# Kernel tuning notes

Hardware: AMD Instinct MI355X
Metric: run time of the kernel (lower is better)

The kernel has to match this reference:

```python
import jax, jax.numpy as jnp
import numpy as np

TEMPERATURE = 0.07
EPS = 1e-12  # F.normalize eps

B, D = 4096, 512

def setup_inputs() -> dict:
    key = jax.random.key(0)
    k1, k2, k3 = jax.random.split(key, 3)
    z1 = jax.random.normal(k1, (B, D), dtype=jnp.float32)
    z2 = jax.random.normal(k2, (B, D), dtype=jnp.float32)
    labels = jax.random.randint(k3, (B,), 0, 10)
    return {"z1": z1, "z2": z2, "labels": labels}

def _normalize(x):
    # F.normalize(x, dim=1): x / max(||x||, eps)
    n = jnp.linalg.norm(x, axis=1, keepdims=True)
    return x / jnp.maximum(n, EPS)

def reference(z1, z2, labels):
    z1 = _normalize(z1)
    z2 = _normalize(z2)
    batch_size = z1.shape[0]
    features = jnp.concatenate([z1, z2], axis=0)  # [2B, D], unit-norm rows
    # cosine similarity of unit vectors == dot product
    similarity = jnp.einsum('id,jd->ij', features, features) / TEMPERATURE  # [2B,2B]
    # positive mask: (i, i+B) and (i+B, i)
    idx = jnp.arange(2 * batch_size)
    pos_idx = jnp.where(idx < batch_size, idx + batch_size, idx - batch_size)
    # log-softmax over rows (diagonal NOT masked, matching the original)
    log_prob = similarity - jax.nn.logsumexp(similarity, axis=1, keepdims=True)
    pos_log_prob = log_prob[idx, pos_idx]  # [2B]
    loss = -jnp.sum(pos_log_prob) / (2 * batch_size)
    return loss
```

## Files before the change

kernel.cpp:

```cpp
#include <hip/hip_runtime.h>
#include <hip/hip_bf16.h>

#define BSZ   4096
#define DIM   512
#define NROW  8192
#define NBLK_NORM (BSZ / 4)
#define INV_T 14.285714285714285f

typedef float f32x4 __attribute__((ext_vector_type(4)));

#define GLOAD_LDS16(gp, lp) __builtin_amdgcn_global_load_lds( \
    (const __attribute__((address_space(1))) unsigned int*)(const void*)(gp), \
    (__attribute__((address_space(3))) unsigned int*)(void*)(lp), 16, 0, 0)

__device__ __forceinline__ unsigned pack_fp8x4(float4 v, float s) {
    int w = 0;
    w = __builtin_amdgcn_cvt_pk_fp8_f32(v.x * s, v.y * s, w, false);
    w = __builtin_amdgcn_cvt_pk_fp8_f32(v.z * s, v.w * s, w, true);
    return (unsigned)w;
}

__global__ __launch_bounds__(256) void nt_norm(const float* __restrict__ z1,
                                               const float* __restrict__ z2,
                                               unsigned char* __restrict__ F,
                                               float* __restrict__ posbuf,
                                               float* __restrict__ rowsum) {
    __shared__ float pd[4];
    const int wid  = threadIdx.x >> 6;
    const int lane = threadIdx.x & 63;
    const int row  = blockIdx.x * 4 + wid;

    if (threadIdx.x < 8) rowsum[blockIdx.x * 8 + threadIdx.x] = 0.0f;

    const float4* a4 = (const float4*)(z1 + (size_t)row * DIM);
    const float4* b4 = (const float4*)(z2 + (size_t)row * DIM);
    float4 a0 = a4[lane], a1 = a4[64 + lane];
    float4 b0 = b4[lane], b1 = b4[64 + lane];

    float s1 = a0.x*a0.x + a0.y*a0.y + a0.z*a0.z + a0.w*a0.w
             + a1.x*a1.x + a1.y*a1.y + a1.z*a1.z + a1.w*a1.w;
    float s2 = b0.x*b0.x + b0.y*b0.y + b0.z*b0.z + b0.w*b0.w
             + b1.x*b1.x + b1.y*b1.y + b1.z*b1.z + b1.w*b1.w;
    float d  = a0.x*b0.x + a0.y*b0.y + a0.z*b0.z + a0.w*b0.w
             + a1.x*b1.x + a1.y*b1.y + a1.z*b1.z + a1.w*b1.w;

    #pragma unroll
    for (int off = 32; off; off >>= 1) {
        s1 += __shfl_xor(s1, off);
        s2 += __shfl_xor(s2, off);
        d  += __shfl_xor(d,  off);
    }

    const float inv1 = 1.0f / fmaxf(sqrtf(s1), 1e-12f);
    const float inv2 = 1.0f / fmaxf(sqrtf(s2), 1e-12f);

    unsigned char* F1 = F + (size_t)row * DIM;
    unsigned char* F2 = F + (size_t)(BSZ + row) * DIM;
    *(unsigned*)(F1 + lane * 4)       = pack_fp8x4(a0, inv1);
    *(unsigned*)(F1 + 256 + lane * 4) = pack_fp8x4(a1, inv1);
    *(unsigned*)(F2 + lane * 4)       = pack_fp8x4(b0, inv2);
    *(unsigned*)(F2 + 256 + lane * 4) = pack_fp8x4(b1, inv2);

    if (lane == 0) pd[wid] = d * inv1 * inv2;
    __syncthreads();
    if (threadIdx.x == 0)
        posbuf[blockIdx.x] = pd[0] + pd[1] + pd[2] + pd[3];
}

__device__ __forceinline__ void stage_fp8(const unsigned char* __restrict__ Ag,
                                          const unsigned char* __restrict__ Bg,
                                          unsigned char* Asb, unsigned char* Bsb,
                                          int tid, int wid) {
    #pragma unroll
    for (int ch = 0; ch < 4; ++ch) {
        const int i   = ch * 256 + tid;
        const int rr  = i >> 3;
        const int cb  = (i & 7) * 16;
        const int src = cb ^ ((rr & 7) << 4);
        const int seg = (ch * 256 + wid * 64) * 16;
        GLOAD_LDS16(Ag + (size_t)rr * DIM + src, Asb + seg);
        GLOAD_LDS16(Bg + (size_t)rr * DIM + src, Bsb + seg);
    }
}

__global__ __launch_bounds__(256, 4) void simexp(const unsigned char* __restrict__ F,
                                                 float* __restrict__ rowsum) {
    __shared__ __align__(16) unsigned char As[2][128 * 128];
    __shared__ __align__(16) unsigned char Bs[2][128 * 128];

    int L = (blockIdx.x & 7) * 260 + (blockIdx.x >> 3);
    int rem = L, s_r = 0;
    for (; s_r < 8; ++s_r) {
        const int rowsz = 36 + 64 * (7 - s_r);
        if (rem < rowsz) break;
        rem -= rowsz;
    }
    int s_c, lr, lc;
    if (rem < 36) {
        s_c = s_r;
        lr = 0;
        while (rem >= 8 - lr) { rem -= 8 - lr; ++lr; }
        lc = lr + rem;
    } else {
        rem -= 36;
        s_c = s_r + 1 + (rem >> 6);
        const int j = rem & 63;
        lr = j >> 3; lc = j & 7;
    }
    const int r = s_r * 8 + lr;
    const int c = s_c * 8 + lc;

    const int tid  = threadIdx.x;
    const int wid  = tid >> 6;
    const int lane = tid & 63;
    const int wr   = wid >> 1;
    const int wc   = wid & 1;
    const size_t row0 = (size_t)r * 128;
    const size_t col0 = (size_t)c * 128;
    const unsigned char* Abase = F + row0 * DIM;
    const unsigned char* Bbase = F + col0 * DIM;

    f32x4 acc[4][4] = {};

    const int rlo = lane & 15;
    const int g8  = (lane >> 4) * 8;
    const int sw  = (lane & 7) << 4;

    stage_fp8(Abase,       Bbase,       As[0], Bs[0], tid, wid);
    stage_fp8(Abase + 128, Bbase + 128, As[1], Bs[1], tid, wid);

    for (int kt = 0; kt < 4; ++kt) {
        const int cur = kt & 1;
        if (kt < 3) asm volatile("s_waitcnt vmcnt(8)" ::: "memory");
        else        asm volatile("s_waitcnt vmcnt(0)" ::: "memory");
        __builtin_amdgcn_s_barrier();

        const unsigned char* Ac = As[cur];
        const unsigned char* Bc = Bs[cur];
        #pragma unroll
        for (int ks = 0; ks < 4; ++ks) {
            const int col = (ks * 32 + g8) ^ sw;
            long a[4], b[4];
            #pragma unroll
            for (int n = 0; n < 4; ++n) {
                const int row = wc * 64 + n * 16 + rlo;
                b[n] = *(const long*)(Bc + row * 128 + col);
            }
            #pragma unroll
            for (int m = 0; m < 4; ++m) {
                const int row = wr * 64 + m * 16 + rlo;
                a[m] = *(const long*)(Ac + row * 128 + col);
            }
            #pragma unroll
            for (int m = 0; m < 4; ++m)
                #pragma unroll
                for (int n = 0; n < 4; ++n)
                    acc[m][n] = __builtin_amdgcn_mfma_f32_16x16x32_fp8_fp8(
                        a[m], b[n], acc[m][n], 0, 0, 0);
        }

        __builtin_amdgcn_s_barrier();
        if (kt + 2 < 4)
            stage_fp8(Abase + (kt + 2) * 128, Bbase + (kt + 2) * 128,
                      As[cur], Bs[cur], tid, wid);
    }

    float p[4][4][4];
    #pragma unroll
    for (int m = 0; m < 4; ++m)
        #pragma unroll
        for (int n = 0; n < 4; ++n)
            #pragma unroll
            for (int j = 0; j < 4; ++j)
                p[m][n][j] = __expf((acc[m][n][j] - 1.0f) * INV_T);

    #pragma unroll
    for (int m = 0; m < 4; ++m)
        #pragma unroll
        for (int j = 0; j < 4; ++j) {
            float rs = p[m][0][j] + p[m][1][j] + p[m][2][j] + p[m][3][j];
            rs += __shfl_xor(rs, 1);
            rs += __shfl_xor(rs, 2);
            rs += __shfl_xor(rs, 4);
            rs += __shfl_xor(rs, 8);
            if ((lane & 15) == 0) {
                const int grow = (int)row0 + wr * 64 + m * 16 + ((lane >> 4) << 2) + j;
                atomicAdd(&rowsum[grow], rs);
            }
        }

    if (r != c) {
        #pragma unroll
        for (int n = 0; n < 4; ++n) {
            float cs = 0.f;
            #pragma unroll
            for (int m = 0; m < 4; ++m)
                #pragma unroll
                for (int j = 0; j < 4; ++j)
                    cs += p[m][n][j];
            cs += __shfl_xor(cs, 16);
            cs += __shfl_xor(cs, 32);
            if (lane < 16) {
                const int gcol = (int)col0 + wc * 64 + n * 16 + lane;
                atomicAdd(&rowsum[gcol], cs);
            }
        }
    }
}

__global__ __launch_bounds__(1024) void nt_final(const float* __restrict__ rowsum,
                                                 const float* __restrict__ posbuf,
                                                 float* __restrict__ out) {
    __shared__ float redl[1024];
    __shared__ float redp[1024];
    float s = 0.f, ps = 0.f;
    for (int i = threadIdx.x; i < NROW; i += 1024) s += logf(rowsum[i]);
    for (int i = threadIdx.x; i < NBLK_NORM; i += 1024) ps += posbuf[i];
    redl[threadIdx.x] = s;
    redp[threadIdx.x] = ps;
    __syncthreads();
    for (int off = 512; off; off >>= 1) {
        if (threadIdx.x < off) {
            redl[threadIdx.x] += redl[threadIdx.x + off];
            redp[threadIdx.x] += redp[threadIdx.x + off];
        }
        __syncthreads();
    }
    if (threadIdx.x == 0) {
        out[0] = INV_T + redl[0] / (float)NROW - redp[0] * INV_T / (float)BSZ;
    }
}

extern "C" void kernel_launch(void* const* d_in, const int* in_sizes, int n_in,
                              void* d_out, int out_size, void* d_ws, size_t ws_size,
                              hipStream_t stream) {
    const float* z1 = (const float*)d_in[0];
    const float* z2 = (const float*)d_in[1];

    unsigned char* F = (unsigned char*)d_ws;
    const size_t FBYTES = (size_t)NROW * DIM;
    float* rowsum = (float*)((char*)d_ws + FBYTES);
    float* posbuf = rowsum + NROW;

    nt_norm<<<dim3(NBLK_NORM), dim3(256), 0, stream>>>(z1, z2, F, posbuf, rowsum);
    simexp<<<dim3(2080), dim3(256), 0, stream>>>(F, rowsum);
    nt_final<<<dim3(1), dim3(1024), 0, stream>>>(rowsum, posbuf, (float*)d_out);
}
```

Measured before the change: 62.55 us.

## Quantize features to FP4 and use scaled MX MFMA for similarity GEMM

Normalized features are quantized to 4-bit e2m1 values with a fixed scale instead of FP8, halving workspace and LDS traffic. The similarity tile uses the 16x16x128 f8f6f4 scaled MFMA with fixed block scales, so each k-tile needs one instruction per output block. Diagonal entries of self tiles are set to exp(0) to correct quantization error on self-similarity. This trades substantial numerical precision for throughput and may exceed the accuracy tolerance.

```diff
diff --git a/kernel.cpp b/kernel.cpp
--- a/kernel.cpp
+++ b/kernel.cpp
@@ -4,20 +4,30 @@
 #define BSZ   4096
 #define DIM   512
 #define NROW  8192
+#define ROWB  256
 #define NBLK_NORM (BSZ / 4)
 #define INV_T 14.285714285714285f
 
-typedef float f32x4 __attribute__((ext_vector_type(4)));
+typedef float f32x4  __attribute__((ext_vector_type(4)));
+typedef int   i32x4v __attribute__((ext_vector_type(4)));
+typedef int   i32x8v __attribute__((ext_vector_type(8)));
 
 #define GLOAD_LDS16(gp, lp) __builtin_amdgcn_global_load_lds( \
     (const __attribute__((address_space(1))) unsigned int*)(const void*)(gp), \
     (__attribute__((address_space(3))) unsigned int*)(void*)(lp), 16, 0, 0)
 
-__device__ __forceinline__ unsigned pack_fp8x4(float4 v, float s) {
-    int w = 0;
-    w = __builtin_amdgcn_cvt_pk_fp8_f32(v.x * s, v.y * s, w, false);
-    w = __builtin_amdgcn_cvt_pk_fp8_f32(v.z * s, v.w * s, w, true);
-    return (unsigned)w;
+__device__ __forceinline__ unsigned q1(float y) {
+    const float a = fabsf(y);
+    unsigned c = (unsigned)(a >= 0.25f) + (unsigned)(a >= 0.75f)
+               + (unsigned)(a >= 1.25f) + (unsigned)(a >= 1.75f)
+               + (unsigned)(a >= 2.5f)  + (unsigned)(a >= 3.5f)
+               + (unsigned)(a >= 5.0f);
+    return c | (y < 0.0f ? 8u : 0u);
+}
+__device__ __forceinline__ unsigned pack8(float4 u, float4 v, float s) {
+    return  q1(u.x * s)        | (q1(u.y * s) << 4)  | (q1(u.z * s) << 8)  |
+           (q1(u.w * s) << 12) | (q1(v.x * s) << 16) | (q1(v.y * s) << 20) |
+           (q1(v.z * s) << 24) | (q1(v.w * s) << 28);
 }
 
 __global__ __launch_bounds__(256) void nt_norm(const float* __restrict__ z1,
@@ -34,8 +44,8 @@
 
     const float4* a4 = (const float4*)(z1 + (size_t)row * DIM);
     const float4* b4 = (const float4*)(z2 + (size_t)row * DIM);
-    float4 a0 = a4[lane], a1 = a4[64 + lane];
-    float4 b0 = b4[lane], b1 = b4[64 + lane];
+    float4 a0 = a4[2 * lane], a1 = a4[2 * lane + 1];
+    float4 b0 = b4[2 * lane], b1 = b4[2 * lane + 1];
 
     float s1 = a0.x*a0.x + a0.y*a0.y + a0.z*a0.z + a0.w*a0.w
              + a1.x*a1.x + a1.y*a1.y + a1.z*a1.z + a1.w*a1.w;
@@ -54,12 +64,8 @@
     const float inv1 = 1.0f / fmaxf(sqrtf(s1), 1e-12f);
     const float inv2 = 1.0f / fmaxf(sqrtf(s2), 1e-12f);
 
-    unsigned char* F1 = F + (size_t)row * DIM;
-    unsigned char* F2 = F + (size_t)(BSZ + row) * DIM;
-    *(unsigned*)(F1 + lane * 4)       = pack_fp8x4(a0, inv1);
-    *(unsigned*)(F1 + 256 + lane * 4) = pack_fp8x4(a1, inv1);
-    *(unsigned*)(F2 + lane * 4)       = pack_fp8x4(b0, inv2);
-    *(unsigned*)(F2 + 256 + lane * 4) = pack_fp8x4(b1, inv2);
+    *(unsigned*)(F + (size_t)row * ROWB + 4 * lane)          = pack8(a0, a1, inv1 * 32.0f);
+    *(unsigned*)(F + (size_t)(BSZ + row) * ROWB + 4 * lane)  = pack8(b0, b1, inv2 * 32.0f);
 
     if (lane == 0) pd[wid] = d * inv1 * inv2;
     __syncthreads();
@@ -67,26 +73,27 @@
         posbuf[blockIdx.x] = pd[0] + pd[1] + pd[2] + pd[3];
 }
 
-__device__ __forceinline__ void stage_fp8(const unsigned char* __restrict__ Ag,
+__device__ __forceinline__ void stage_fp4(const unsigned char* __restrict__ Ag,
                                           const unsigned char* __restrict__ Bg,
                                           unsigned char* Asb, unsigned char* Bsb,
-                                          int tid, int wid) {
-    #pragma unroll
-    for (int ch = 0; ch < 4; ++ch) {
-        const int i   = ch * 256 + tid;
-        const int rr  = i >> 3;
-        const int cb  = (i & 7) * 16;
-        const int src = cb ^ ((rr & 7) << 4);
-        const int seg = (ch * 256 + wid * 64) * 16;
-        GLOAD_LDS16(Ag + (size_t)rr * DIM + src, Asb + seg);
-        GLOAD_LDS16(Bg + (size_t)rr * DIM + src, Bsb + seg);
+                                          int kt, int tid) {
+    #pragma unroll
+    for (int ch = 0; ch < 2; ++ch) {
+        const int i    = ch * 256 + tid;
+        const int rr   = i >> 2;
+        const int slot = i & 3;
+        const int sg   = slot ^ ((rr >> 1) & 3);
+        const int dst  = i * 16;
+        const size_t go = (size_t)rr * ROWB + kt * 64 + sg * 16;
+        GLOAD_LDS16(Ag + go, Asb + dst);
+        GLOAD_LDS16(Bg + go, Bsb + dst);
     }
 }
 
 __global__ __launch_bounds__(256, 4) void simexp(const unsigned char* __restrict__ F,
                                                  float* __restrict__ rowsum) {
-    __shared__ __align__(16) unsigned char As[2][128 * 128];
-    __shared__ __align__(16) unsigned char Bs[2][128 * 128];
+    __shared__ __align__(16) unsigned char As[2][128 * 64];
+    __shared__ __align__(16) unsigned char Bs[2][128 * 64];
 
     int L = (blockIdx.x & 7) * 260 + (blockIdx.x >> 3);
     int rem = L, s_r = 0;
@@ -117,52 +124,51 @@
     const int wc   = wid & 1;
     const size_t row0 = (size_t)r * 128;
     const size_t col0 = (size_t)c * 128;
-    const unsigned char* Abase = F + row0 * DIM;
-    const unsigned char* Bbase = F + col0 * DIM;
+    const unsigned char* Abase = F + row0 * ROWB;
+    const unsigned char* Bbase = F + col0 * ROWB;
 
     f32x4 acc[4][4] = {};
 
-    const int rlo = lane & 15;
-    const int g8  = (lane >> 4) * 8;
-    const int sw  = (lane & 7) << 4;
-
-    stage_fp8(Abase,       Bbase,       As[0], Bs[0], tid, wid);
-    stage_fp8(Abase + 128, Bbase + 128, As[1], Bs[1], tid, wid);
+    const int rlo  = lane & 15;
+    const int hi   = lane >> 4;
+    const int fcol = (hi ^ ((lane >> 1) & 3)) << 4;
+
+    stage_fp4(Abase, Bbase, As[0], Bs[0], 0, tid);
+    stage_fp4(Abase, Bbase, As[1], Bs[1], 1, tid);
 
     for (int kt = 0; kt < 4; ++kt) {
         const int cur = kt & 1;
-        if (kt < 3) asm volatile("s_waitcnt vmcnt(8)" ::: "memory");
+        if (kt < 3) asm volatile("s_waitcnt vmcnt(4)" ::: "memory");
         else        asm volatile("s_waitcnt vmcnt(0)" ::: "memory");
         __builtin_amdgcn_s_barrier();
 
         const unsigned char* Ac = As[cur];
         const unsigned char* Bc = Bs[cur];
-        #pragma unroll
-        for (int ks = 0; ks < 4; ++ks) {
-            const int col = (ks * 32 + g8) ^ sw;
-            long a[4], b[4];
-            #pragma unroll
-            for (int n = 0; n < 4; ++n) {
-                const int row = wc * 64 + n * 16 + rlo;
-                b[n] = *(const long*)(Bc + row * 128 + col);
-            }
-            #pragma unroll
-            for (int m = 0; m < 4; ++m) {
-                const int row = wr * 64 + m * 16 + rlo;
-                a[m] = *(const long*)(Ac + row * 128 + col);
-            }
-            #pragma unroll
-            for (int m = 0; m < 4; ++m)
-                #pragma unroll
-                for (int n = 0; n < 4; ++n)
-                    acc[m][n] = __builtin_amdgcn_mfma_f32_16x16x32_fp8_fp8(
-                        a[m], b[n], acc[m][n], 0, 0, 0);
-        }
-
-        __builtin_amdgcn_s_barrier();
-        if (kt + 2 < 4)
-            stage_fp8(Abase + (kt + 2) * 128, Bbase + (kt + 2) * 128,
-                      As[cur], Bs[cur], tid, wid);
+
+        i32x8v b8[4];
+        #pragma unroll
+        for (int n = 0; n < 4; ++n) {
+            b8[n] = (i32x8v){0, 0, 0, 0, 0, 0, 0, 0};
+            i32x4v t = *(const i32x4v*)(Bc + (wc * 64 + n * 16 + rlo) * 64 + fcol);
+            b8[n][0] = t[0]; b8[n][1] = t[1]; b8[n][2] = t[2]; b8[n][3] = t[3];
+        }
+        i32x8v a8 = (i32x8v){0, 0, 0, 0, 0, 0, 0, 0};
+        #pragma unroll
+        for (int m = 0; m < 4; ++m) {
+            i32x4v t = *(const i32x4v*)(Ac + (wr * 64 + m * 16 + rlo) * 64 + fcol);
+            a8[0] = t[0]; a8[1] = t[1]; a8[2] = t[2]; a8[3] = t[3];
+            #pragma unroll
+            for (int n = 0; n < 4; ++n)
+                acc[m][n] = __builtin_amdgcn_mfma_scale_f32_16x16x128_f8f6f4(
+                    a8, b8[n], acc[m][n], 4, 4,
+                    0, 122,
+                    0, 122);
+        }
+
+        if (kt < 2) {
+            __builtin_amdgcn_s_barrier();
+            stage_fp4(Abase, Bbase, As[cur], Bs[cur], kt + 2, tid);
+        }
     }
 
     float p[4][4][4];
@@ -173,6 +179,15 @@
             #pragma unroll
             for (int j = 0; j < 4; ++j)
                 p[m][n][j] = __expf((acc[m][n][j] - 1.0f) * INV_T);
+
+    if (r == c && wr == wc) {
+        const int jd = (lane & 15) - (hi << 2);
+        if (jd >= 0 && jd < 4) {
+            #pragma unroll
+            for (int m = 0; m < 4; ++m)
+                p[m][m][jd] = 1.0f;
+        }
+    }
 
     #pragma unroll
     for (int m = 0; m < 4; ++m)
@@ -184,7 +199,7 @@
             rs += __shfl_xor(rs, 4);
             rs += __shfl_xor(rs, 8);
             if ((lane & 15) == 0) {
-                const int grow = (int)row0 + wr * 64 + m * 16 + ((lane >> 4) << 2) + j;
+                const int grow = (int)row0 + wr * 64 + m * 16 + (hi << 2) + j;
                 atomicAdd(&rowsum[grow], rs);
             }
         }
@@ -238,7 +253,7 @@
     const float* z2 = (const float*)d_in[1];
 
     unsigned char* F = (unsigned char*)d_ws;
-    const size_t FBYTES = (size_t)NROW * DIM;
+    const size_t FBYTES = (size_t)NROW * ROWB;
     float* rowsum = (float*)((char*)d_ws + FBYTES);
     float* posbuf = rowsum + NROW;
 
```

Result: slower. 75.46 us (+20.6%).
